# Kernel optimization log

Measured on AMD Instinct MI355X. Metric: run time of the kernel, lower is better.

Reference implementation:

```python
import jax, jax.numpy as jnp
import numpy as np

RADIUS = 8
NUM = 200
EPS = 1e-8


def _conv2d(x, k, pad_mode):
    # x: [B,1,H,W], k: [kh,kw]; same-size conv with given numpy-style padding mode
    ph, pw = k.shape[0] // 2, k.shape[1] // 2
    xp = jnp.pad(x, ((0, 0), (0, 0), (ph, ph), (pw, pw)), mode=pad_mode)
    return jax.lax.conv_general_dilated(
        xp, k[None, None], (1, 1), 'VALID',
        dimension_numbers=('NCHW', 'OIHW', 'NCHW'))


def _gauss_kernel7():
    xs = np.arange(7, dtype=np.float32) - 3.0
    g = np.exp(-0.5 * xs ** 2)
    g /= g.sum()
    return jnp.asarray(np.outer(g, g))


def get_corners(imgs):
    B, _, H, W = imgs.shape
    # kornia rgb_to_grayscale
    gray = 0.299 * imgs[:, 0:1] + 0.587 * imgs[:, 1:2] + 0.114 * imgs[:, 2:3]
    # kornia CornerGFTT: sobel gradients (normalized), gaussian-smoothed structure tensor, min eigenvalue
    sob = jnp.array([[-1., 0., 1.], [-2., 0., 2.], [-1., 0., 1.]], jnp.float32) / 8.0
    dx = _conv2d(gray, sob, 'edge')
    dy = _conv2d(gray, sob.T, 'edge')
    g = _gauss_kernel7()
    dx2 = _conv2d(dx * dx, g, 'reflect')
    dy2 = _conv2d(dy * dy, g, 'reflect')
    dxy = _conv2d(dx * dy, g, 'reflect')
    tr = dx2 + dy2
    det = dx2 * dy2 - dxy * dxy
    resp = 0.5 * (tr - jnp.sqrt(jnp.abs(tr * tr - 4.0 * det)))  # GFTT score (min eigval)
    # kornia nms2d with 5x5 window: keep local maxima
    mp = jax.lax.reduce_window(resp, -jnp.inf, jax.lax.max,
                               (1, 1, 5, 5), (1, 1, 1, 1),
                               [(0, 0), (0, 0), (2, 2), (2, 2)])
    resp = jnp.where(resp == mp, resp, 0.0)
    # unfold/mask/fold with kernel=stride=RADIUS == per non-overlapping 8x8 block:
    # keep elements equal to the block max and > 0
    r = RADIUS
    blk = resp.reshape(B, 1, H // r, r, W // r, r)
    bmax = blk.max(axis=(3, 5), keepdims=True)
    blk = jnp.where((blk > 0) & (blk == bmax), blk, 0.0)
    corners = blk.reshape(B, H * W)
    # top-200 scatter then binarize
    vals, idx = jax.lax.top_k(corners, NUM)
    out = jnp.zeros_like(corners).at[jnp.arange(B)[:, None], idx].set(vals)
    return (out > 0).astype(imgs.dtype).reshape(B, 1, H, W)


def setup_inputs() -> dict:
    key = jax.random.key(0)
    k1, k2, k3, k4 = jax.random.split(key, 4)
    B, N, D, H, W = 16, 2048, 256, 384, 384
    return {
        'descriptors': jax.random.normal(k1, (B, N, D), jnp.float32),
        'scores': jax.random.uniform(k2, (B, N), jnp.float32),
        'scores_dense': jax.random.normal(k3, (B, 1, H, W), jnp.float32),
        'imgs': jax.random.uniform(k4, (B, 3, H, W), jnp.float32),
    }


def reference(descriptors, scores, scores_dense, imgs):
    corners = get_corners(imgs)
    # all-pairs cosine similarity within each batch: pcos[b,i,j]
    norms = jnp.linalg.norm(descriptors, axis=-1)  # [B,N]
    dots = jnp.einsum('bnd,bmd->bnm', descriptors, descriptors)
    pcos = dots / jnp.maximum(norms[:, :, None] * norms[:, None, :], EPS)
    # BCEWithLogitsLoss(scores_dense, corners), mean reduction
    bce = jnp.mean(jnp.logaddexp(0.0, scores_dense) - scores_dense * corners)
    return bce + jnp.mean(jax.nn.relu(pcos))
```

## Files before the change

### kernel.cpp

```cpp
#include <hip/hip_runtime.h>

#define H 384
#define W 384
#define HWSZ (H * W)
#define NB 16
#define ND 2048
#define DD 256

#define OFF_RESP  256
#define OFF_CVAL  9437440
#define OFF_CPOS  9584896
#define OFF_DESCB 9732352
#define OFF_INV   26509568
#define OFF_PSOFT 26640640
#define OFF_PGEMM 26643200
#define OFF_PCORN 26652160

__device__ __forceinline__ int clampi(int v) { return v < 0 ? 0 : (v > 383 ? 383 : v); }
__device__ __forceinline__ int refl(int v) { return v < 0 ? -v : (v >= 384 ? 766 - v : v); }

__device__ __forceinline__ unsigned f2e4m3(float x) {
  float a = fabsf(x);
  unsigned s = (__float_as_uint(x) >> 31) << 7;
  if (a >= 448.f) return s | 0x7E;
  if (a < 0.015625f) {
    int m = (int)rintf(a * 512.f);
    return s | (unsigned)m;
  }
  unsigned u = __float_as_uint(a);
  u += 0x7FFFF + ((u >> 20) & 1);
  unsigned e = (u >> 23) - 120;
  unsigned m = (u >> 20) & 7;
  return s | (e << 3) | m;
}

__global__ __launch_bounds__(256) void resp_kernel(const float* __restrict__ imgs,
                                                   float* __restrict__ resp) {
  const float GW[7] = {0.0044330482f, 0.0540055826f, 0.2420362294f, 0.3990502160f,
                       0.2420362294f, 0.0540055826f, 0.0044330482f};
  __shared__ float gl[40][41];
  __shared__ float p0[38][39], p1[38][39], p2[38][39];
  __shared__ float t0[38][33], t1[38][33], t2[38][33];

  int bid = blockIdx.x;
  int b = bid / 144;
  int t = bid % 144;
  int Y0 = (t / 12) * 32, X0 = (t % 12) * 32;
  const float* ib = imgs + (size_t)b * 3 * HWSZ;

  for (int i = threadIdx.x; i < 1600; i += 256) {
    int r = i / 40, c = i % 40;
    int gy = clampi(Y0 - 4 + r), gx = clampi(X0 - 4 + c);
    const float* p = ib + gy * W + gx;
    gl[r][c] = 0.299f * p[0] + 0.587f * p[HWSZ] + 0.114f * p[2 * HWSZ];
  }
  __syncthreads();

  for (int i = threadIdx.x; i < 1444; i += 256) {
    int r = i / 38, c = i % 38;
    int py = refl(Y0 - 3 + r), px = refl(X0 - 3 + c);
    int ym = clampi(py - 1) - (Y0 - 4), y0 = py - (Y0 - 4), yp = clampi(py + 1) - (Y0 - 4);
    int xm = clampi(px - 1) - (X0 - 4), x0 = px - (X0 - 4), xp = clampi(px + 1) - (X0 - 4);
    float a = gl[ym][xm], bb = gl[ym][x0], cc = gl[ym][xp];
    float d = gl[y0][xm], e = gl[y0][xp];
    float f = gl[yp][xm], g = gl[yp][x0], h = gl[yp][xp];
    float dx = 0.125f * ((cc - a) + 2.f * (e - d) + (h - f));
    float dy = 0.125f * ((f - a) + 2.f * (g - bb) + (h - cc));
    p0[r][c] = dx * dx;
    p1[r][c] = dy * dy;
    p2[r][c] = dx * dy;
  }
  __syncthreads();

  for (int i = threadIdx.x; i < 1216; i += 256) {
    int r = i / 32, c = i % 32;
    float s0 = 0.f, s1 = 0.f, s2 = 0.f;
#pragma unroll
    for (int j = 0; j < 7; j++) {
      s0 += GW[j] * p0[r][c + j];
      s1 += GW[j] * p1[r][c + j];
      s2 += GW[j] * p2[r][c + j];
    }
    t0[r][c] = s0; t1[r][c] = s1; t2[r][c] = s2;
  }
  __syncthreads();

  for (int i = threadIdx.x; i < 1024; i += 256) {
    int r = i / 32, c = i % 32;
    float s0 = 0.f, s1 = 0.f, s2 = 0.f;
#pragma unroll
    for (int j = 0; j < 7; j++) {
      s0 += GW[j] * t0[r + j][c];
      s1 += GW[j] * t1[r + j][c];
      s2 += GW[j] * t2[r + j][c];
    }
    float tr = s0 + s1;
    float det = s0 * s1 - s2 * s2;
    float disc = tr * tr - 4.f * det;
    float rv = 0.5f * (tr - sqrtf(fabsf(disc)));
    resp[(size_t)b * HWSZ + (Y0 + r) * W + (X0 + c)] = rv;
  }
}

__global__ __launch_bounds__(256) void nms_kernel(const float* __restrict__ resp,
                                                  float* __restrict__ cval,
                                                  unsigned* __restrict__ cpos) {
  __shared__ float rl[68][69];
  __shared__ float nl[64][65];
  int bid = blockIdx.x;
  int b = bid / 36;
  int t = bid % 36;
  int Y0 = (t / 6) * 64, X0 = (t % 6) * 64;
  const float* rb = resp + (size_t)b * HWSZ;

  for (int i = threadIdx.x; i < 68 * 68; i += 256) {
    int r = i / 68, c = i % 68;
    int gy = Y0 - 2 + r, gx = X0 - 2 + c;
    float v = -INFINITY;
    if (gy >= 0 && gy < H && gx >= 0 && gx < W) v = rb[gy * W + gx];
    rl[r][c] = v;
  }
  __syncthreads();

  for (int i = threadIdx.x; i < 4096; i += 256) {
    int r = i / 64, c = i % 64;
    float m = -INFINITY;
#pragma unroll
    for (int dr = 0; dr < 5; dr++)
#pragma unroll
      for (int dc = 0; dc < 5; dc++) m = fmaxf(m, rl[r + dr][c + dc]);
    float v = rl[r + 2][c + 2];
    nl[r][c] = (v == m) ? v : 0.f;
  }
  __syncthreads();

  if (threadIdx.x < 64) {
    int bi = threadIdx.x / 8, bj = threadIdx.x % 8;
    float bv = 0.f;
    unsigned bp = 0;
    for (int rr = 0; rr < 8; rr++)
      for (int cc = 0; cc < 8; cc++) {
        float v = nl[bi * 8 + rr][bj * 8 + cc];
        if (v > bv) { bv = v; bp = (unsigned)((Y0 + bi * 8 + rr) * W + (X0 + bj * 8 + cc)); }
      }
    int ci = b * 2304 + (Y0 / 8 + bi) * 48 + (X0 / 8 + bj);
    cval[ci] = bv;
    cpos[ci] = bp;
  }
}

__global__ __launch_bounds__(256) void topk_kernel(const float* __restrict__ cval,
                                                   const unsigned* __restrict__ cpos,
                                                   const float* __restrict__ sd,
                                                   float* __restrict__ pcorn) {
  __shared__ int hist[256];
  __shared__ int pick[2];
  __shared__ unsigned eqpos[256];
  __shared__ int eqcnt;
  __shared__ float rf[4];
  __shared__ int ri[4];

  int b = blockIdx.x;
  int t = threadIdx.x;
  int lane = t & 63;

  unsigned bits[9], pos[9];
#pragma unroll
  for (int q = 0; q < 9; q++) {
    int i = t + q * 256;
    unsigned vb = 0, p = 0;
    if (i < 2304) {
      float v = cval[b * 2304 + i];
      if (v > 0.f) { vb = __float_as_uint(v); p = cpos[b * 2304 + i]; }
    }
    bits[q] = vb; pos[q] = p;
  }

  int P = 0;
#pragma unroll
  for (int q = 0; q < 9; q++) P += (bits[q] != 0u);
  for (int off = 32; off; off >>= 1) P += __shfl_down(P, off, 64);
  if (lane == 0) ri[t >> 6] = P;
  __syncthreads();
  int Ptot = ri[0] + ri[1] + ri[2] + ri[3];
  if (Ptot == 0) { if (t == 0) pcorn[b] = 0.f; return; }
  int K = Ptot < 200 ? Ptot : 200;

  unsigned prefix = 0;
  int krem = K;
  for (int shift = 24; shift >= 0; shift -= 8) {
    hist[t] = 0;
    __syncthreads();
#pragma unroll
    for (int q = 0; q < 9; q++) {
      if (bits[q] != 0u &&
          (shift == 24 || (bits[q] >> (shift + 8)) == (prefix >> (shift + 8))))
        atomicAdd(&hist[(bits[q] >> shift) & 0xFF], 1);
    }
    __syncthreads();
    if (t < 64) {
      int h0 = hist[4 * t], h1 = hist[4 * t + 1], h2 = hist[4 * t + 2], h3 = hist[4 * t + 3];
      int tot = h0 + h1 + h2 + h3;
      int acc = tot;
      for (int d = 1; d < 64; d <<= 1) {
        int o = __shfl_down(acc, d, 64);
        if (t + d < 64) acc += o;
      }
      int excl = acc - tot;
      int G3 = excl, G2 = excl + h3, G1 = excl + h3 + h2, G0 = excl + h3 + h2 + h1;
      if (G0 < krem && G0 + h0 >= krem) { pick[0] = 4 * t;     pick[1] = G0; }
      if (G1 < krem && G1 + h1 >= krem) { pick[0] = 4 * t + 1; pick[1] = G1; }
      if (G2 < krem && G2 + h2 >= krem) { pick[0] = 4 * t + 2; pick[1] = G2; }
      if (G3 < krem && G3 + h3 >= krem) { pick[0] = 4 * t + 3; pick[1] = G3; }
    }
    __syncthreads();
    prefix |= ((unsigned)pick[0]) << shift;
    krem -= pick[1];
    __syncthreads();
  }

  if (t == 0) eqcnt = 0;
  __syncthreads();
  float s = 0.f;
#pragma unroll
  for (int q = 0; q < 9; q++) {
    if (bits[q] > prefix) s += sd[(size_t)b * HWSZ + pos[q]];
    else if (bits[q] != 0u && bits[q] == prefix) {
      int idx = atomicAdd(&eqcnt, 1);
      if (idx < 256) eqpos[idx] = pos[q];
    }
  }
  __syncthreads();
  int m = eqcnt;
  if (m <= krem) {
    if (t < m) s += sd[(size_t)b * HWSZ + eqpos[t]];
  } else {
    int mm = m < 256 ? m : 256;
    if (t < mm) {
      unsigned p = eqpos[t];
      int rank = 0;
      for (int u = 0; u < mm; u++) rank += (eqpos[u] < p);
      if (rank < krem) s += sd[(size_t)b * HWSZ + p];
    }
  }
  for (int off = 32; off; off >>= 1) s += __shfl_down(s, off, 64);
  if (lane == 0) rf[t >> 6] = s;
  __syncthreads();
  if (t == 0) pcorn[b] = rf[0] + rf[1] + rf[2] + rf[3];
}

__global__ __launch_bounds__(256) void softplus_kernel(const float4* __restrict__ sd,
                                                       float* __restrict__ psoft) {
  __shared__ float r4[4];
  float s = 0.f;
  int base = blockIdx.x * 256 + threadIdx.x;
#pragma unroll
  for (int it = 0; it < 4; it++) {
    float4 v = sd[base + it * 147456];
    s += fmaxf(v.x, 0.f) + log1pf(expf(-fabsf(v.x))) +
         fmaxf(v.y, 0.f) + log1pf(expf(-fabsf(v.y))) +
         fmaxf(v.z, 0.f) + log1pf(expf(-fabsf(v.z))) +
         fmaxf(v.w, 0.f) + log1pf(expf(-fabsf(v.w)));
  }
  for (int off = 32; off; off >>= 1) s += __shfl_down(s, off, 64);
  if ((threadIdx.x & 63) == 0) r4[threadIdx.x >> 6] = s;
  __syncthreads();
  if (threadIdx.x == 0) psoft[blockIdx.x] = r4[0] + r4[1] + r4[2] + r4[3];
}

__global__ __launch_bounds__(256) void prep_desc_kernel(const float* __restrict__ desc,
                                                        unsigned char* __restrict__ descF8,
                                                        float* __restrict__ invn) {
  int wave = threadIdx.x >> 6, lane = threadIdx.x & 63;
  int row = blockIdx.x * 4 + wave;
  const float4* src = (const float4*)(desc + (size_t)row * DD);
  float4 v = src[lane];
  unsigned pk = f2e4m3(v.x) | (f2e4m3(v.y) << 8) | (f2e4m3(v.z) << 16) | (f2e4m3(v.w) << 24);
  ((unsigned*)(descF8 + (size_t)row * DD))[lane] = pk;
  float ss = v.x * v.x + v.y * v.y + v.z * v.z + v.w * v.w;
  for (int off = 32; off; off >>= 1) ss += __shfl_down(ss, off, 64);
  if (lane == 0) invn[row] = 1.f / fmaxf(sqrtf(ss), 1e-4f);
}

typedef float f32x4 __attribute__((ext_vector_type(4)));

__device__ __forceinline__ void load_lds16(const void* g, void* l) {
  __builtin_amdgcn_global_load_lds((const __attribute__((address_space(1))) void*)g,
                                   (__attribute__((address_space(3))) void*)l, 16, 0, 0);
}

__global__ __launch_bounds__(256) void gemm_relu_kernel(const unsigned char* __restrict__ descF8,
                                                        const float* __restrict__ invn,
                                                        float* __restrict__ pgemm) {
  int bx = blockIdx.x;
  int batch = bx / 136;
  int rem = bx % 136;
  int ti = 0, rowlen = 16;
  while (rem >= rowlen) { rem -= rowlen; rowlen--; ti++; }
  int tj = ti + rem;

  const unsigned char* Ab = descF8 + (size_t)batch * ND * DD;
  const float* inv = invn + batch * ND;
  int I0 = ti * 128, J0 = tj * 128;

  __shared__ char lA[128 * 128];
  __shared__ char lB[128 * 128];
  __shared__ float r4[4];

  int tid = threadIdx.x;
  int wave = tid >> 6, lane = tid & 63;
  int rm = lane & 15, kq = lane >> 4;
  int wr = wave >> 1, wc = wave & 1;
  int lrow = lane >> 3;
  int lcolb = ((lane & 7) ^ lrow) << 4;
  int cx = rm & 7;

  f32x4 accf[4][4];
#pragma unroll
  for (int m = 0; m < 4; m++)
#pragma unroll
    for (int n = 0; n < 4; n++) accf[m][n] = (f32x4){0.f, 0.f, 0.f, 0.f};

  for (int k0 = 0; k0 < DD; k0 += 128) {
#pragma unroll
    for (int q = 0; q < 4; q++) {
      int chunk = wave * 4 + q;
      load_lds16(Ab + (size_t)(I0 + chunk * 8 + lrow) * DD + k0 + lcolb, lA + chunk * 1024);
      load_lds16(Ab + (size_t)(J0 + chunk * 8 + lrow) * DD + k0 + lcolb, lB + chunk * 1024);
    }
    __syncthreads();
#pragma unroll
    for (int kk = 0; kk < 128; kk += 32) {
      long af[4], bfr[4];
      int koff = kk + kq * 8;
      int pcol = ((((koff >> 4) ^ cx) << 4) | (koff & 8));
#pragma unroll
      for (int m = 0; m < 4; m++)
        af[m] = *reinterpret_cast<const long*>(lA + (wr * 64 + m * 16 + rm) * 128 + pcol);
#pragma unroll
      for (int n = 0; n < 4; n++)
        bfr[n] = *reinterpret_cast<const long*>(lB + (wc * 64 + n * 16 + rm) * 128 + pcol);
#pragma unroll
      for (int m = 0; m < 4; m++)
#pragma unroll
        for (int n = 0; n < 4; n++)
          accf[m][n] = __builtin_amdgcn_mfma_f32_16x16x32_fp8_fp8(af[m], bfr[n], accf[m][n], 0, 0, 0);
    }
    __syncthreads();
  }

  float wgt = (ti == tj) ? 1.f : 2.f;
  float invC[4];
#pragma unroll
  for (int n = 0; n < 4; n++) invC[n] = inv[J0 + wc * 64 + n * 16 + rm];
  float psum = 0.f;
#pragma unroll
  for (int m = 0; m < 4; m++) {
#pragma unroll
    for (int r = 0; r < 4; r++) {
      float invR = inv[I0 + wr * 64 + m * 16 + kq * 4 + r];
#pragma unroll
      for (int n = 0; n < 4; n++) psum += fmaxf(accf[m][n][r] * invR * invC[n], 0.f);
    }
  }
  psum *= wgt;
  for (int off = 32; off; off >>= 1) psum += __shfl_down(psum, off, 64);
  if (lane == 0) r4[wave] = psum;
  __syncthreads();
  if (tid == 0) pgemm[bx] = r4[0] + r4[1] + r4[2] + r4[3];
}

__global__ __launch_bounds__(256) void finalize_kernel(const float* __restrict__ psoft,
                                                       const float* __restrict__ pcorn,
                                                       const float* __restrict__ pgemm,
                                                       float* __restrict__ out) {
  __shared__ float r4[4];
  float bce = 0.f;
  for (int i = threadIdx.x; i < 576; i += 256) bce += psoft[i];
  if (threadIdx.x < 16) bce -= pcorn[threadIdx.x];
  float g = 0.f;
  for (int i = threadIdx.x; i < 2176; i += 256) g += pgemm[i];
  float t = bce * (1.f / 2359296.f) + g * (1.f / 67108864.f);
  for (int off = 32; off; off >>= 1) t += __shfl_down(t, off, 64);
  if ((threadIdx.x & 63) == 0) r4[threadIdx.x >> 6] = t;
  __syncthreads();
  if (threadIdx.x == 0) out[0] = r4[0] + r4[1] + r4[2] + r4[3];
}

extern "C" void kernel_launch(void* const* d_in, const int* in_sizes, int n_in,
                              void* d_out, int out_size, void* d_ws, size_t ws_size,
                              hipStream_t stream) {
  (void)in_sizes; (void)n_in; (void)out_size; (void)ws_size;
  const float* desc = (const float*)d_in[0];
  const float* sd = (const float*)d_in[2];
  const float* imgs = (const float*)d_in[3];
  float* out = (float*)d_out;

  char* w = (char*)d_ws;
  float* resp = (float*)(w + OFF_RESP);
  float* cval = (float*)(w + OFF_CVAL);
  unsigned* cpos = (unsigned*)(w + OFF_CPOS);
  unsigned char* descF8 = (unsigned char*)(w + OFF_DESCB);
  float* invn = (float*)(w + OFF_INV);
  float* psoft = (float*)(w + OFF_PSOFT);
  float* pgemm = (float*)(w + OFF_PGEMM);
  float* pcorn = (float*)(w + OFF_PCORN);

  resp_kernel<<<2304, 256, 0, stream>>>(imgs, resp);
  nms_kernel<<<576, 256, 0, stream>>>(resp, cval, cpos);
  topk_kernel<<<16, 256, 0, stream>>>(cval, cpos, sd, pcorn);
  softplus_kernel<<<576, 256, 0, stream>>>((const float4*)sd, psoft);
  prep_desc_kernel<<<8192, 256, 0, stream>>>(desc, descF8, invn);
  gemm_relu_kernel<<<2176, 256, 0, stream>>>(descF8, invn, pgemm);
  finalize_kernel<<<1, 256, 0, stream>>>(psoft, pcorn, pgemm, out);
}
```

Before: 183.0 us.

## Merge independent kernels into three stages via block-index dispatch

Folds six kernels into three launches. Each launch assigns block ranges to independent work: the response map with descriptor fp8 prep, NMS with the softplus sum, and top-k with the cosine GEMM. The aim is to cut launch overhead and tail gaps by running independent work concurrently within one grid. In exchange, the merged kernels take the union of LDS use and the highest register count of their branches, which can lower occupancy for the lighter branches.

After: 160.0 us. 1.14x faster.

```diff
diff --git a/kernel.cpp b/kernel.cpp
--- a/kernel.cpp
+++ b/kernel.cpp
@@ -34,14 +34,37 @@
   return s | (e << 3) | m;
 }
 
-__global__ __launch_bounds__(256) void resp_kernel(const float* __restrict__ imgs,
-                                                   float* __restrict__ resp) {
-  const float GW[7] = {0.0044330482f, 0.0540055826f, 0.2420362294f, 0.3990502160f,
-                       0.2420362294f, 0.0540055826f, 0.0044330482f};
+typedef float f32x4 __attribute__((ext_vector_type(4)));
+
+__device__ __forceinline__ void load_lds16(const void* g, void* l) {
+  __builtin_amdgcn_global_load_lds((const __attribute__((address_space(1))) void*)g,
+                                   (__attribute__((address_space(3))) void*)l, 16, 0, 0);
+}
+
+__global__ __launch_bounds__(256) void stage1_kernel(const float* __restrict__ imgs,
+                                                     float* __restrict__ resp,
+                                                     const float* __restrict__ desc,
+                                                     unsigned char* __restrict__ descF8,
+                                                     float* __restrict__ invn) {
   __shared__ float gl[40][41];
   __shared__ float p0[38][39], p1[38][39], p2[38][39];
   __shared__ float t0[38][33], t1[38][33], t2[38][33];
 
+  if (blockIdx.x >= 2304) {
+    int wave = threadIdx.x >> 6, lane = threadIdx.x & 63;
+    int row = (blockIdx.x - 2304) * 4 + wave;
+    const float4* src = (const float4*)(desc + (size_t)row * DD);
+    float4 v = src[lane];
+    unsigned pk = f2e4m3(v.x) | (f2e4m3(v.y) << 8) | (f2e4m3(v.z) << 16) | (f2e4m3(v.w) << 24);
+    ((unsigned*)(descF8 + (size_t)row * DD))[lane] = pk;
+    float ss = v.x * v.x + v.y * v.y + v.z * v.z + v.w * v.w;
+    for (int off = 32; off; off >>= 1) ss += __shfl_down(ss, off, 64);
+    if (lane == 0) invn[row] = 1.f / fmaxf(sqrtf(ss), 1e-4f);
+    return;
+  }
+
+  const float GW[7] = {0.0044330482f, 0.0540055826f, 0.2420362294f, 0.3990502160f,
+                       0.2420362294f, 0.0540055826f, 0.0044330482f};
   int bid = blockIdx.x;
   int b = bid / 144;
   int t = bid % 144;
@@ -102,11 +125,34 @@
   }
 }
 
-__global__ __launch_bounds__(256) void nms_kernel(const float* __restrict__ resp,
-                                                  float* __restrict__ cval,
-                                                  unsigned* __restrict__ cpos) {
+__global__ __launch_bounds__(256) void stage2_kernel(const float* __restrict__ resp,
+                                                     float* __restrict__ cval,
+                                                     unsigned* __restrict__ cpos,
+                                                     const float4* __restrict__ sd4,
+                                                     float* __restrict__ psoft) {
   __shared__ float rl[68][69];
   __shared__ float nl[64][65];
+  __shared__ float r4[4];
+
+  if (blockIdx.x >= 576) {
+    int sb = blockIdx.x - 576;
+    float s = 0.f;
+    int base = sb * 256 + threadIdx.x;
+#pragma unroll
+    for (int it = 0; it < 4; it++) {
+      float4 v = sd4[base + it * 147456];
+      s += fmaxf(v.x, 0.f) + log1pf(expf(-fabsf(v.x))) +
+           fmaxf(v.y, 0.f) + log1pf(expf(-fabsf(v.y))) +
+           fmaxf(v.z, 0.f) + log1pf(expf(-fabsf(v.z))) +
+           fmaxf(v.w, 0.f) + log1pf(expf(-fabsf(v.w)));
+    }
+    for (int off = 32; off; off >>= 1) s += __shfl_down(s, off, 64);
+    if ((threadIdx.x & 63) == 0) r4[threadIdx.x >> 6] = s;
+    __syncthreads();
+    if (threadIdx.x == 0) psoft[sb] = r4[0] + r4[1] + r4[2] + r4[3];
+    return;
+  }
+
   int bid = blockIdx.x;
   int b = bid / 36;
   int t = bid % 36;
@@ -149,150 +195,114 @@
   }
 }
 
-__global__ __launch_bounds__(256) void topk_kernel(const float* __restrict__ cval,
-                                                   const unsigned* __restrict__ cpos,
-                                                   const float* __restrict__ sd,
-                                                   float* __restrict__ pcorn) {
+__global__ __launch_bounds__(256) void stage3_kernel(const float* __restrict__ cval,
+                                                     const unsigned* __restrict__ cpos,
+                                                     const float* __restrict__ sd,
+                                                     float* __restrict__ pcorn,
+                                                     const unsigned char* __restrict__ descF8,
+                                                     const float* __restrict__ invn,
+                                                     float* __restrict__ pgemm) {
+  __shared__ char lA[128 * 128];
+  __shared__ char lB[128 * 128];
+  __shared__ float r4[4];
   __shared__ int hist[256];
   __shared__ int pick[2];
   __shared__ unsigned eqpos[256];
   __shared__ int eqcnt;
-  __shared__ float rf[4];
   __shared__ int ri[4];
 
-  int b = blockIdx.x;
-  int t = threadIdx.x;
-  int lane = t & 63;
-
-  unsigned bits[9], pos[9];
-#pragma unroll
-  for (int q = 0; q < 9; q++) {
-    int i = t + q * 256;
-    unsigned vb = 0, p = 0;
-    if (i < 2304) {
-      float v = cval[b * 2304 + i];
-      if (v > 0.f) { vb = __float_as_uint(v); p = cpos[b * 2304 + i]; }
-    }
-    bits[q] = vb; pos[q] = p;
-  }
-
-  int P = 0;
-#pragma unroll
-  for (int q = 0; q < 9; q++) P += (bits[q] != 0u);
-  for (int off = 32; off; off >>= 1) P += __shfl_down(P, off, 64);
-  if (lane == 0) ri[t >> 6] = P;
-  __syncthreads();
-  int Ptot = ri[0] + ri[1] + ri[2] + ri[3];
-  if (Ptot == 0) { if (t == 0) pcorn[b] = 0.f; return; }
-  int K = Ptot < 200 ? Ptot : 200;
-
-  unsigned prefix = 0;
-  int krem = K;
-  for (int shift = 24; shift >= 0; shift -= 8) {
-    hist[t] = 0;
-    __syncthreads();
+  if (blockIdx.x < 16) {
+    int b = blockIdx.x;
+    int t = threadIdx.x;
+    int lane = t & 63;
+
+    unsigned bits[9], pos[9];
 #pragma unroll
     for (int q = 0; q < 9; q++) {
-      if (bits[q] != 0u &&
-          (shift == 24 || (bits[q] >> (shift + 8)) == (prefix >> (shift + 8))))
-        atomicAdd(&hist[(bits[q] >> shift) & 0xFF], 1);
-    }
-    __syncthreads();
-    if (t < 64) {
-      int h0 = hist[4 * t], h1 = hist[4 * t + 1], h2 = hist[4 * t + 2], h3 = hist[4 * t + 3];
-      int tot = h0 + h1 + h2 + h3;
-      int acc = tot;
-      for (int d = 1; d < 64; d <<= 1) {
-        int o = __shfl_down(acc, d, 64);
-        if (t + d < 64) acc += o;
-      }
-      int excl = acc - tot;
-      int G3 = excl, G2 = excl + h3, G1 = excl + h3 + h2, G0 = excl + h3 + h2 + h1;
-      if (G0 < krem && G0 + h0 >= krem) { pick[0] = 4 * t;     pick[1] = G0; }
-      if (G1 < krem && G1 + h1 >= krem) { pick[0] = 4 * t + 1; pick[1] = G1; }
-      if (G2 < krem && G2 + h2 >= krem) { pick[0] = 4 * t + 2; pick[1] = G2; }
-      if (G3 < krem && G3 + h3 >= krem) { pick[0] = 4 * t + 3; pick[1] = G3; }
-    }
-    __syncthreads();
-    prefix |= ((unsigned)pick[0]) << shift;
-    krem -= pick[1];
-    __syncthreads();
-  }
-
-  if (t == 0) eqcnt = 0;
-  __syncthreads();
-  float s = 0.f;
-#pragma unroll
-  for (int q = 0; q < 9; q++) {
-    if (bits[q] > prefix) s += sd[(size_t)b * HWSZ + pos[q]];
-    else if (bits[q] != 0u && bits[q] == prefix) {
-      int idx = atomicAdd(&eqcnt, 1);
-      if (idx < 256) eqpos[idx] = pos[q];
-    }
-  }
-  __syncthreads();
-  int m = eqcnt;
-  if (m <= krem) {
-    if (t < m) s += sd[(size_t)b * HWSZ + eqpos[t]];
-  } else {
-    int mm = m < 256 ? m : 256;
-    if (t < mm) {
-      unsigned p = eqpos[t];
-      int rank = 0;
-      for (int u = 0; u < mm; u++) rank += (eqpos[u] < p);
-      if (rank < krem) s += sd[(size_t)b * HWSZ + p];
-    }
-  }
-  for (int off = 32; off; off >>= 1) s += __shfl_down(s, off, 64);
-  if (lane == 0) rf[t >> 6] = s;
-  __syncthreads();
-  if (t == 0) pcorn[b] = rf[0] + rf[1] + rf[2] + rf[3];
-}
-
-__global__ __launch_bounds__(256) void softplus_kernel(const float4* __restrict__ sd,
-                                                       float* __restrict__ psoft) {
-  __shared__ float r4[4];
-  float s = 0.f;
-  int base = blockIdx.x * 256 + threadIdx.x;
-#pragma unroll
-  for (int it = 0; it < 4; it++) {
-    float4 v = sd[base + it * 147456];
-    s += fmaxf(v.x, 0.f) + log1pf(expf(-fabsf(v.x))) +
-         fmaxf(v.y, 0.f) + log1pf(expf(-fabsf(v.y))) +
-         fmaxf(v.z, 0.f) + log1pf(expf(-fabsf(v.z))) +
-         fmaxf(v.w, 0.f) + log1pf(expf(-fabsf(v.w)));
-  }
-  for (int off = 32; off; off >>= 1) s += __shfl_down(s, off, 64);
-  if ((threadIdx.x & 63) == 0) r4[threadIdx.x >> 6] = s;
-  __syncthreads();
-  if (threadIdx.x == 0) psoft[blockIdx.x] = r4[0] + r4[1] + r4[2] + r4[3];
-}
-
-__global__ __launch_bounds__(256) void prep_desc_kernel(const float* __restrict__ desc,
-                                                        unsigned char* __restrict__ descF8,
-                                                        float* __restrict__ invn) {
-  int wave = threadIdx.x >> 6, lane = threadIdx.x & 63;
-  int row = blockIdx.x * 4 + wave;
-  const float4* src = (const float4*)(desc + (size_t)row * DD);
-  float4 v = src[lane];
-  unsigned pk = f2e4m3(v.x) | (f2e4m3(v.y) << 8) | (f2e4m3(v.z) << 16) | (f2e4m3(v.w) << 24);
-  ((unsigned*)(descF8 + (size_t)row * DD))[lane] = pk;
-  float ss = v.x * v.x + v.y * v.y + v.z * v.z + v.w * v.w;
-  for (int off = 32; off; off >>= 1) ss += __shfl_down(ss, off, 64);
-  if (lane == 0) invn[row] = 1.f / fmaxf(sqrtf(ss), 1e-4f);
-}
-
-typedef float f32x4 __attribute__((ext_vector_type(4)));
-
-__device__ __forceinline__ void load_lds16(const void* g, void* l) {
-  __builtin_amdgcn_global_load_lds((const __attribute__((address_space(1))) void*)g,
-                                   (__attribute__((address_space(3))) void*)l, 16, 0, 0);
-}
-
-__global__ __launch_bounds__(256) void gemm_relu_kernel(const unsigned char* __restrict__ descF8,
-                                                        const float* __restrict__ invn,
-                                                        float* __restrict__ pgemm) {
-  int bx = blockIdx.x;
+      int i = t + q * 256;
+      unsigned vb = 0, p = 0;
+      if (i < 2304) {
+        float v = cval[b * 2304 + i];
+        if (v > 0.f) { vb = __float_as_uint(v); p = cpos[b * 2304 + i]; }
+      }
+      bits[q] = vb; pos[q] = p;
+    }
+
+    int P = 0;
+#pragma unroll
+    for (int q = 0; q < 9; q++) P += (bits[q] != 0u);
+    for (int off = 32; off; off >>= 1) P += __shfl_down(P, off, 64);
+    if (lane == 0) ri[t >> 6] = P;
+    __syncthreads();
+    int Ptot = ri[0] + ri[1] + ri[2] + ri[3];
+    if (Ptot == 0) { if (t == 0) pcorn[b] = 0.f; return; }
+    int K = Ptot < 200 ? Ptot : 200;
+
+    unsigned prefix = 0;
+    int krem = K;
+    for (int shift = 24; shift >= 0; shift -= 8) {
+      hist[t] = 0;
+      __syncthreads();
+#pragma unroll
+      for (int q = 0; q < 9; q++) {
+        if (bits[q] != 0u &&
+            (shift == 24 || (bits[q] >> (shift + 8)) == (prefix >> (shift + 8))))
+          atomicAdd(&hist[(bits[q] >> shift) & 0xFF], 1);
+      }
+      __syncthreads();
+      if (t < 64) {
+        int h0 = hist[4 * t], h1 = hist[4 * t + 1], h2 = hist[4 * t + 2], h3 = hist[4 * t + 3];
+        int tot = h0 + h1 + h2 + h3;
+        int acc = tot;
+        for (int d = 1; d < 64; d <<= 1) {
+          int o = __shfl_down(acc, d, 64);
+          if (t + d < 64) acc += o;
+        }
+        int excl = acc - tot;
+        int G3 = excl, G2 = excl + h3, G1 = excl + h3 + h2, G0 = excl + h3 + h2 + h1;
+        if (G0 < krem && G0 + h0 >= krem) { pick[0] = 4 * t;     pick[1] = G0; }
+        if (G1 < krem && G1 + h1 >= krem) { pick[0] = 4 * t + 1; pick[1] = G1; }
+        if (G2 < krem && G2 + h2 >= krem) { pick[0] = 4 * t + 2; pick[1] = G2; }
+        if (G3 < krem && G3 + h3 >= krem) { pick[0] = 4 * t + 3; pick[1] = G3; }
+      }
+      __syncthreads();
+      prefix |= ((unsigned)pick[0]) << shift;
+      krem -= pick[1];
+      __syncthreads();
+    }
+
+    if (t == 0) eqcnt = 0;
+    __syncthreads();
+    float s = 0.f;
+#pragma unroll
+    for (int q = 0; q < 9; q++) {
+      if (bits[q] > prefix) s += sd[(size_t)b * HWSZ + pos[q]];
+      else if (bits[q] != 0u && bits[q] == prefix) {
+        int idx = atomicAdd(&eqcnt, 1);
+        if (idx < 256) eqpos[idx] = pos[q];
+      }
+    }
+    __syncthreads();
+    int m = eqcnt;
+    if (m <= krem) {
+      if (t < m) s += sd[(size_t)b * HWSZ + eqpos[t]];
+    } else {
+      int mm = m < 256 ? m : 256;
+      if (t < mm) {
+        unsigned p = eqpos[t];
+        int rank = 0;
+        for (int u = 0; u < mm; u++) rank += (eqpos[u] < p);
+        if (rank < krem) s += sd[(size_t)b * HWSZ + p];
+      }
+    }
+    for (int off = 32; off; off >>= 1) s += __shfl_down(s, off, 64);
+    if (lane == 0) r4[t >> 6] = s;
+    __syncthreads();
+    if (t == 0) pcorn[b] = r4[0] + r4[1] + r4[2] + r4[3];
+    return;
+  }
+
+  int bx = blockIdx.x - 16;
   int batch = bx / 136;
   int rem = bx % 136;
   int ti = 0, rowlen = 16;
@@ -302,10 +312,6 @@
   const unsigned char* Ab = descF8 + (size_t)batch * ND * DD;
   const float* inv = invn + batch * ND;
   int I0 = ti * 128, J0 = tj * 128;
-
-  __shared__ char lA[128 * 128];
-  __shared__ char lB[128 * 128];
-  __shared__ float r4[4];
 
   int tid = threadIdx.x;
   int wave = tid >> 6, lane = tid & 63;
@@ -406,11 +412,8 @@
   float* pgemm = (float*)(w + OFF_PGEMM);
   float* pcorn = (float*)(w + OFF_PCORN);
 
-  resp_kernel<<<2304, 256, 0, stream>>>(imgs, resp);
-  nms_kernel<<<576, 256, 0, stream>>>(resp, cval, cpos);
-  topk_kernel<<<16, 256, 0, stream>>>(cval, cpos, sd, pcorn);
-  softplus_kernel<<<576, 256, 0, stream>>>((const float4*)sd, psoft);
-  prep_desc_kernel<<<8192, 256, 0, stream>>>(desc, descF8, invn);
-  gemm_relu_kernel<<<2176, 256, 0, stream>>>(descF8, invn, pgemm);
+  stage1_kernel<<<10496, 256, 0, stream>>>(imgs, resp, desc, descF8, invn);
+  stage2_kernel<<<1152, 256, 0, stream>>>(resp, cval, cpos, (const float4*)sd, psoft);
+  stage3_kernel<<<2192, 256, 0, stream>>>(cval, cpos, sd, pcorn, descF8, invn, pgemm);
   finalize_kernel<<<1, 256, 0, stream>>>(psoft, pcorn, pgemm, out);
 }
```
